# Kernel tuning notes

Hardware: AMD Instinct MI355X
Metric: run time of the kernel (lower is better)

The kernel has to match this reference:

```python
import jax, jax.numpy as jnp
import numpy as np

B, N_IN, N_MF, N_RULES, N_OUT_MEM, N_OUT = 16384, 6, 5, 2048, 12, 2
TANH_CENTERS = np.array([0.0, 0.75], dtype=np.float32)
TANH_SCALE = np.array([4.0, 0.75], dtype=np.float32)
EPS = 1e-12


def setup_inputs() -> dict:
    key = jax.random.key(0)
    k = jax.random.split(key, 6)
    x = jax.random.normal(k[0], (B, N_IN), dtype=jnp.float32)
    mf_centers = jax.random.normal(k[1], (N_IN, N_MF), dtype=jnp.float32)
    # strictly positive widths for the Gaussian memberships
    mf_scales = jax.random.uniform(k[2], (N_IN, N_MF), dtype=jnp.float32) + 0.5
    out_centers = jax.random.normal(k[3], (N_OUT_MEM,), dtype=jnp.float32)
    input_rules = jax.random.randint(k[4], (N_RULES, N_IN), 0, N_IN * N_MF, dtype=jnp.int32)
    output_rules = jax.random.randint(k[5], (N_RULES, N_OUT), 0, N_OUT_MEM, dtype=jnp.int32)
    return {"x": x, "mf_centers": mf_centers, "mf_scales": mf_scales,
            "out_centers": out_centers, "input_rules": input_rules,
            "output_rules": output_rules}


def reference(x, mf_centers, mf_scales, out_centers, input_rules, output_rules):
    # fuzzify: Gaussian membership per (input var, MF) -> [B, N_IN*N_MF]
    z = (x[:, :, None] - mf_centers[None]) / mf_scales[None]      # [B, N_IN, N_MF]
    fuzzified = jnp.exp(-z * z).reshape(x.shape[0], -1)           # [B, 30]
    # rules: gather antecedent memberships, min t-norm over antecedents
    gathered = fuzzified[:, input_rules]                          # [B, R, N_IN]
    weights = jnp.min(gathered, axis=2)                           # [B, R]
    # L1 normalize across rules (F.normalize p=1, dim=1)
    l1 = jnp.sum(jnp.abs(weights), axis=1, keepdims=True)
    normalized = weights / jnp.maximum(l1, EPS)
    # defuzzify: gather output-membership centers per rule, then matmul
    ow = out_centers[output_rules]                                # [R, N_OUT]
    defuzz = normalized @ ow                                      # [B, N_OUT]
    # constrain scaling
    return jnp.tanh(defuzz) * jnp.asarray(TANH_SCALE) + jnp.asarray(TANH_CENTERS)
```

## Files before the change

kernel.cpp:

```cpp
#include <hip/hip_runtime.h>
#include <hip/hip_bf16.h>

#define BATCH      16384
#define N_IN       6
#define N_MF       5
#define N_FUZZ     30
#define N_RULES    2048
#define N_OUT_MEM  12

#define ROWS_PB    256
#define SPLITS     4
#define RULES_PB   (N_RULES / SPLITS)
#define THREADS    1024
#define WAVES      16
#define RULES_PW   (RULES_PB / WAVES)
#define ROWGROUPS  (BATCH / ROWS_PB)

#define WS_PACKED_OFF  0
#define WS_OW_OFF      8192
#define WS_PART_OFF    24576

typedef _Float16 f16x2 __attribute__((ext_vector_type(2)));

__device__ inline int probe_is_bf16(const void* mfs) {
    const unsigned int* w = (const unsigned int*)mfs;
    int ok = 1;
    for (int k = 0; k < 15; ++k) {
        const unsigned int v = w[k];
        const float lo = __uint_as_float(v << 16);
        const float hi = __uint_as_float(v & 0xffff0000u);
        if (!(lo >= 0.4f && lo <= 1.6f && hi >= 0.4f && hi <= 1.6f)) { ok = 0; break; }
    }
    return ok;
}

__global__ void anfis_prep(const int* __restrict__ input_rules,
                           const int* __restrict__ output_rules,
                           const void* __restrict__ oc_,
                           const void* __restrict__ mfs_,
                           unsigned int* __restrict__ packed,
                           float2* __restrict__ ow) {
    __shared__ int flag;
    if (threadIdx.x == 0) flag = probe_is_bf16(mfs_);
    __syncthreads();
    const bool is_bf16 = (flag != 0);

    const int r = blockIdx.x * blockDim.x + threadIdx.x;
    if (r >= N_RULES) return;
    const int* rp = input_rules + r * N_IN;
    unsigned int p = 0;
#pragma unroll
    for (int i = 0; i < N_IN; ++i) p |= ((unsigned int)rp[i] & 31u) << (5 * i);
    packed[r] = p;

    const int o0i = output_rules[2 * r + 0];
    const int o1i = output_rules[2 * r + 1];
    float o0, o1;
    if (is_bf16) {
        const unsigned short* oc = (const unsigned short*)oc_;
        o0 = __uint_as_float((unsigned int)oc[o0i] << 16);
        o1 = __uint_as_float((unsigned int)oc[o1i] << 16);
    } else {
        const float* oc = (const float*)oc_;
        o0 = oc[o0i]; o1 = oc[o1i];
    }
    ow[r] = make_float2(o0, o1);
}

__global__ __launch_bounds__(THREADS, 4)
void anfis_main(const void* __restrict__ x_,
                const void* __restrict__ mfc_,
                const void* __restrict__ mfs_,
                const unsigned int* __restrict__ packed,
                const float2* __restrict__ ow,
                float* __restrict__ partials) {
    __shared__ float xs[ROWS_PB * N_IN];
    __shared__ float2 cinv[N_FUZZ];
    __shared__ uint2 fuzz4[N_FUZZ][64];
    __shared__ float pl1[WAVES][ROWS_PB];
    __shared__ float pd0[WAVES][ROWS_PB];
    __shared__ float pd1[WAVES][ROWS_PB];
    __shared__ int flag;

    const int t     = threadIdx.x;
    const int g     = blockIdx.x >> 2;
    const int split = blockIdx.x & 3;
    const int row0  = g * ROWS_PB;

    if (t == 0) flag = probe_is_bf16(mfs_);
    __syncthreads();
    const bool is_bf16 = (flag != 0);

    if (is_bf16) {
        const unsigned short* xp = (const unsigned short*)x_ + row0 * N_IN;
        for (int i = t; i < ROWS_PB * N_IN; i += THREADS)
            xs[i] = __uint_as_float((unsigned int)xp[i] << 16);
    } else {
        const float* xp = (const float*)x_ + row0 * N_IN;
        for (int i = t; i < ROWS_PB * N_IN; i += THREADS) xs[i] = xp[i];
    }
    if (t < N_FUZZ) {
        float c, s;
        if (is_bf16) {
            c = __uint_as_float((unsigned int)((const unsigned short*)mfc_)[t] << 16);
            s = __uint_as_float((unsigned int)((const unsigned short*)mfs_)[t] << 16);
        } else {
            c = ((const float*)mfc_)[t];
            s = ((const float*)mfs_)[t];
        }
        cinv[t] = make_float2(c, 1.0f / s);
    }
    __syncthreads();

    for (int e = t; e < N_FUZZ * 64; e += THREADS) {
        const int v    = e >> 6;
        const int lane = e & 63;
        const int i    = v / N_MF;
        const float2 ci = cinv[v];
        float f[4];
#pragma unroll
        for (int k = 0; k < 4; ++k) {
            const float z = (xs[(lane + 64 * k) * N_IN + i] - ci.x) * ci.y;
            f[k] = __expf(-z * z);
        }
        f16x2 a = { (_Float16)f[0], (_Float16)f[1] };
        f16x2 b = { (_Float16)f[2], (_Float16)f[3] };
        uint2 u;
        u.x = __builtin_bit_cast(unsigned int, a);
        u.y = __builtin_bit_cast(unsigned int, b);
        fuzz4[v][lane] = u;
    }
    __syncthreads();

    const int lane = t & 63;
    const int wave = __builtin_amdgcn_readfirstlane(t >> 6);
    const uint2* fz = &fuzz4[0][0];

    float l1[4] = {0.f, 0.f, 0.f, 0.f};
    float d0[4] = {0.f, 0.f, 0.f, 0.f};
    float d1[4] = {0.f, 0.f, 0.f, 0.f};

    const int rbase = split * RULES_PB + wave * RULES_PW;
#pragma unroll 4
    for (int j = 0; j < RULES_PW; ++j) {
        const int r = rbase + j;
        const unsigned int p = packed[r];
        const float2 o = ow[r];
        const uint2 g0 = fz[((p      ) & 31u) * 64 + lane];
        const uint2 g1 = fz[((p >> 5 ) & 31u) * 64 + lane];
        const uint2 g2 = fz[((p >> 10) & 31u) * 64 + lane];
        const uint2 g3 = fz[((p >> 15) & 31u) * 64 + lane];
        const uint2 g4 = fz[((p >> 20) & 31u) * 64 + lane];
        const uint2 g5 = fz[((p >> 25) & 31u) * 64 + lane];
        f16x2 wa = __builtin_elementwise_min(__builtin_bit_cast(f16x2, g0.x),
                                             __builtin_bit_cast(f16x2, g1.x));
        wa = __builtin_elementwise_min(wa, __builtin_bit_cast(f16x2, g2.x));
        wa = __builtin_elementwise_min(wa, __builtin_bit_cast(f16x2, g3.x));
        wa = __builtin_elementwise_min(wa, __builtin_bit_cast(f16x2, g4.x));
        wa = __builtin_elementwise_min(wa, __builtin_bit_cast(f16x2, g5.x));
        f16x2 wb = __builtin_elementwise_min(__builtin_bit_cast(f16x2, g0.y),
                                             __builtin_bit_cast(f16x2, g1.y));
        wb = __builtin_elementwise_min(wb, __builtin_bit_cast(f16x2, g2.y));
        wb = __builtin_elementwise_min(wb, __builtin_bit_cast(f16x2, g3.y));
        wb = __builtin_elementwise_min(wb, __builtin_bit_cast(f16x2, g4.y));
        wb = __builtin_elementwise_min(wb, __builtin_bit_cast(f16x2, g5.y));
        const float w0 = (float)wa.x, w1 = (float)wa.y;
        const float w2 = (float)wb.x, w3 = (float)wb.y;
        l1[0] += w0; d0[0] += w0 * o.x; d1[0] += w0 * o.y;
        l1[1] += w1; d0[1] += w1 * o.x; d1[1] += w1 * o.y;
        l1[2] += w2; d0[2] += w2 * o.x; d1[2] += w2 * o.y;
        l1[3] += w3; d0[3] += w3 * o.x; d1[3] += w3 * o.y;
    }
#pragma unroll
    for (int k = 0; k < 4; ++k) {
        pl1[wave][lane + 64 * k] = l1[k];
        pd0[wave][lane + 64 * k] = d0[k];
        pd1[wave][lane + 64 * k] = d1[k];
    }
    __syncthreads();

    if (t < ROWS_PB) {
        float a = 0.f, b = 0.f, c = 0.f;
#pragma unroll
        for (int wv = 0; wv < WAVES; ++wv) {
            a += pl1[wv][t];
            b += pd0[wv][t];
            c += pd1[wv][t];
        }
        const int row = row0 + t;
        partials[(split * 3 + 0) * BATCH + row] = a;
        partials[(split * 3 + 1) * BATCH + row] = b;
        partials[(split * 3 + 2) * BATCH + row] = c;
    }
}

__global__ void anfis_finalize(const float* __restrict__ partials,
                               const void* __restrict__ mfs_,
                               void* __restrict__ out_) {
    __shared__ int flag;
    if (threadIdx.x == 0) flag = probe_is_bf16(mfs_);
    __syncthreads();
    const int row = blockIdx.x * blockDim.x + threadIdx.x;
    if (row >= BATCH) return;
    float l1 = 0.f, d0 = 0.f, d1 = 0.f;
#pragma unroll
    for (int s = 0; s < SPLITS; ++s) {
        l1 += partials[(s * 3 + 0) * BATCH + row];
        d0 += partials[(s * 3 + 1) * BATCH + row];
        d1 += partials[(s * 3 + 2) * BATCH + row];
    }
    const float inv = 1.0f / fmaxf(l1, 1e-12f);
    const float y0 = tanhf(d0 * inv) * 4.00f + 0.00f;
    const float y1 = tanhf(d1 * inv) * 0.75f + 0.75f;
    if (flag) {
        __hip_bfloat162 o;
        o.x = __float2bfloat16(y0);
        o.y = __float2bfloat16(y1);
        ((__hip_bfloat162*)out_)[row] = o;
    } else {
        ((float2*)out_)[row] = make_float2(y0, y1);
    }
}

extern "C" void kernel_launch(void* const* d_in, const int* in_sizes, int n_in,
                              void* d_out, int out_size, void* d_ws, size_t ws_size,
                              hipStream_t stream) {
    (void)in_sizes; (void)n_in; (void)out_size; (void)ws_size;
    const void* x_   = d_in[0];
    const void* mfc_ = d_in[1];
    const void* mfs_ = d_in[2];
    const void* oc_  = d_in[3];
    const int* input_rules  = (const int*)d_in[4];
    const int* output_rules = (const int*)d_in[5];

    unsigned int* packed = (unsigned int*)((char*)d_ws + WS_PACKED_OFF);
    float2*       ow     = (float2*)((char*)d_ws + WS_OW_OFF);
    float*        parts  = (float*)((char*)d_ws + WS_PART_OFF);

    anfis_prep<<<(N_RULES + 255) / 256, 256, 0, stream>>>(
        input_rules, output_rules, oc_, mfs_, packed, ow);

    anfis_main<<<ROWGROUPS * SPLITS, THREADS, 0, stream>>>(
        x_, mfc_, mfs_, packed, ow, parts);

    anfis_finalize<<<BATCH / 256, 256, 0, stream>>>(parts, mfs_, d_out);
}
```

Baseline: 80.96 us.

## Fuse prep, main and finalize kernels using last-block atomic reduction

Merges the three launches into one kernel. Each block packs its split's rule indices and output weights into LDS, so the separate prep kernel and its global round trip go away. The last of the four split blocks for a row group, found with an atomic counter, sums the partials and applies tanh, replacing the finalize kernel. In exchange every block now redoes rule preprocessing, and the change adds a memset plus threadfence/atomic synchronisation.

```diff
diff --git a/kernel.cpp b/kernel.cpp
--- a/kernel.cpp
+++ b/kernel.cpp
@@ -16,9 +16,8 @@
 #define RULES_PW   (RULES_PB / WAVES)
 #define ROWGROUPS  (BATCH / ROWS_PB)
 
-#define WS_PACKED_OFF  0
-#define WS_OW_OFF      8192
-#define WS_PART_OFF    24576
+#define WS_PART_OFF  0
+#define WS_CNT_OFF   (SPLITS * 3 * BATCH * 4)
 
 typedef _Float16 f16x2 __attribute__((ext_vector_type(2)));
 
@@ -34,53 +33,26 @@
     return ok;
 }
 
-__global__ void anfis_prep(const int* __restrict__ input_rules,
-                           const int* __restrict__ output_rules,
-                           const void* __restrict__ oc_,
-                           const void* __restrict__ mfs_,
-                           unsigned int* __restrict__ packed,
-                           float2* __restrict__ ow) {
-    __shared__ int flag;
-    if (threadIdx.x == 0) flag = probe_is_bf16(mfs_);
-    __syncthreads();
-    const bool is_bf16 = (flag != 0);
-
-    const int r = blockIdx.x * blockDim.x + threadIdx.x;
-    if (r >= N_RULES) return;
-    const int* rp = input_rules + r * N_IN;
-    unsigned int p = 0;
-#pragma unroll
-    for (int i = 0; i < N_IN; ++i) p |= ((unsigned int)rp[i] & 31u) << (5 * i);
-    packed[r] = p;
-
-    const int o0i = output_rules[2 * r + 0];
-    const int o1i = output_rules[2 * r + 1];
-    float o0, o1;
-    if (is_bf16) {
-        const unsigned short* oc = (const unsigned short*)oc_;
-        o0 = __uint_as_float((unsigned int)oc[o0i] << 16);
-        o1 = __uint_as_float((unsigned int)oc[o1i] << 16);
-    } else {
-        const float* oc = (const float*)oc_;
-        o0 = oc[o0i]; o1 = oc[o1i];
-    }
-    ow[r] = make_float2(o0, o1);
-}
-
 __global__ __launch_bounds__(THREADS, 4)
-void anfis_main(const void* __restrict__ x_,
-                const void* __restrict__ mfc_,
-                const void* __restrict__ mfs_,
-                const unsigned int* __restrict__ packed,
-                const float2* __restrict__ ow,
-                float* __restrict__ partials) {
-    __shared__ float xs[ROWS_PB * N_IN];
-    __shared__ float2 cinv[N_FUZZ];
-    __shared__ uint2 fuzz4[N_FUZZ][64];
-    __shared__ float pl1[WAVES][ROWS_PB];
-    __shared__ float pd0[WAVES][ROWS_PB];
-    __shared__ float pd1[WAVES][ROWS_PB];
-    __shared__ int flag;
+void anfis_fused(const void* __restrict__ x_,
+                 const void* __restrict__ mfc_,
+                 const void* __restrict__ mfs_,
+                 const void* __restrict__ oc_,
+                 const int*  __restrict__ input_rules,
+                 const int*  __restrict__ output_rules,
+                 float* __restrict__ partials,
+                 int*   __restrict__ counters,
+                 void*  __restrict__ out_) {
+    __shared__ float        xs[ROWS_PB * N_IN];
+    __shared__ float2       cinv[N_FUZZ];
+    __shared__ uint2        fuzz4[N_FUZZ][64];
+    __shared__ unsigned int packed_lds[RULES_PB];
+    __shared__ float2       ow_lds[RULES_PB];
+    __shared__ float        pl1[WAVES][ROWS_PB];
+    __shared__ float        pd0[WAVES][ROWS_PB];
+    __shared__ float        pd1[WAVES][ROWS_PB];
+    __shared__ int          flag;
+    __shared__ int          amLast;
 
     const int t     = threadIdx.x;
     const int g     = blockIdx.x >> 2;
@@ -90,6 +62,27 @@
     if (t == 0) flag = probe_is_bf16(mfs_);
     __syncthreads();
     const bool is_bf16 = (flag != 0);
+
+    for (int r2 = t; r2 < RULES_PB; r2 += THREADS) {
+        const int r = split * RULES_PB + r2;
+        const int* rp = input_rules + r * N_IN;
+        unsigned int p = 0;
+#pragma unroll
+        for (int i = 0; i < N_IN; ++i) p |= ((unsigned int)rp[i] & 31u) << (5 * i);
+        packed_lds[r2] = p;
+        const int o0i = output_rules[2 * r + 0];
+        const int o1i = output_rules[2 * r + 1];
+        float o0, o1;
+        if (is_bf16) {
+            const unsigned short* oc = (const unsigned short*)oc_;
+            o0 = __uint_as_float((unsigned int)oc[o0i] << 16);
+            o1 = __uint_as_float((unsigned int)oc[o1i] << 16);
+        } else {
+            const float* oc = (const float*)oc_;
+            o0 = oc[o0i]; o1 = oc[o1i];
+        }
+        ow_lds[r2] = make_float2(o0, o1);
+    }
 
     if (is_bf16) {
         const unsigned short* xp = (const unsigned short*)x_ + row0 * N_IN;
@@ -140,12 +133,12 @@
     float d0[4] = {0.f, 0.f, 0.f, 0.f};
     float d1[4] = {0.f, 0.f, 0.f, 0.f};
 
-    const int rbase = split * RULES_PB + wave * RULES_PW;
+    const int rbase = wave * RULES_PW;
 #pragma unroll 4
     for (int j = 0; j < RULES_PW; ++j) {
-        const int r = rbase + j;
-        const unsigned int p = packed[r];
-        const float2 o = ow[r];
+        const int r2 = rbase + j;
+        const unsigned int p = packed_lds[r2];
+        const float2 o = ow_lds[r2];
         const uint2 g0 = fz[((p      ) & 31u) * 64 + lane];
         const uint2 g1 = fz[((p >> 5 ) & 31u) * 64 + lane];
         const uint2 g2 = fz[((p >> 10) & 31u) * 64 + lane];
@@ -192,33 +185,36 @@
         partials[(split * 3 + 1) * BATCH + row] = b;
         partials[(split * 3 + 2) * BATCH + row] = c;
     }
-}
-
-__global__ void anfis_finalize(const float* __restrict__ partials,
-                               const void* __restrict__ mfs_,
-                               void* __restrict__ out_) {
-    __shared__ int flag;
-    if (threadIdx.x == 0) flag = probe_is_bf16(mfs_);
-    __syncthreads();
-    const int row = blockIdx.x * blockDim.x + threadIdx.x;
-    if (row >= BATCH) return;
-    float l1 = 0.f, d0 = 0.f, d1 = 0.f;
-#pragma unroll
-    for (int s = 0; s < SPLITS; ++s) {
-        l1 += partials[(s * 3 + 0) * BATCH + row];
-        d0 += partials[(s * 3 + 1) * BATCH + row];
-        d1 += partials[(s * 3 + 2) * BATCH + row];
-    }
-    const float inv = 1.0f / fmaxf(l1, 1e-12f);
-    const float y0 = tanhf(d0 * inv) * 4.00f + 0.00f;
-    const float y1 = tanhf(d1 * inv) * 0.75f + 0.75f;
-    if (flag) {
-        __hip_bfloat162 o;
-        o.x = __float2bfloat16(y0);
-        o.y = __float2bfloat16(y1);
-        ((__hip_bfloat162*)out_)[row] = o;
-    } else {
-        ((float2*)out_)[row] = make_float2(y0, y1);
+    __threadfence();
+    if (t == 0) {
+        const int old = atomicAdd(&counters[g], 1);
+        amLast = (old == SPLITS - 1);
+    }
+    __syncthreads();
+
+    if (amLast) {
+        __threadfence();
+        if (t < ROWS_PB) {
+            const int row = row0 + t;
+            float l1s = 0.f, d0s = 0.f, d1s = 0.f;
+#pragma unroll
+            for (int s = 0; s < SPLITS; ++s) {
+                l1s += partials[(s * 3 + 0) * BATCH + row];
+                d0s += partials[(s * 3 + 1) * BATCH + row];
+                d1s += partials[(s * 3 + 2) * BATCH + row];
+            }
+            const float inv = 1.0f / fmaxf(l1s, 1e-12f);
+            const float y0 = tanhf(d0s * inv) * 4.00f + 0.00f;
+            const float y1 = tanhf(d1s * inv) * 0.75f + 0.75f;
+            if (is_bf16) {
+                __hip_bfloat162 o;
+                o.x = __float2bfloat16(y0);
+                o.y = __float2bfloat16(y1);
+                ((__hip_bfloat162*)out_)[row] = o;
+            } else {
+                ((float2*)out_)[row] = make_float2(y0, y1);
+            }
+        }
     }
 }
 
@@ -226,22 +222,13 @@
                               void* d_out, int out_size, void* d_ws, size_t ws_size,
                               hipStream_t stream) {
     (void)in_sizes; (void)n_in; (void)out_size; (void)ws_size;
-    const void* x_   = d_in[0];
-    const void* mfc_ = d_in[1];
-    const void* mfs_ = d_in[2];
-    const void* oc_  = d_in[3];
-    const int* input_rules  = (const int*)d_in[4];
-    const int* output_rules = (const int*)d_in[5];
-
-    unsigned int* packed = (unsigned int*)((char*)d_ws + WS_PACKED_OFF);
-    float2*       ow     = (float2*)((char*)d_ws + WS_OW_OFF);
-    float*        parts  = (float*)((char*)d_ws + WS_PART_OFF);
-
-    anfis_prep<<<(N_RULES + 255) / 256, 256, 0, stream>>>(
-        input_rules, output_rules, oc_, mfs_, packed, ow);
-
-    anfis_main<<<ROWGROUPS * SPLITS, THREADS, 0, stream>>>(
-        x_, mfc_, mfs_, packed, ow, parts);
-
-    anfis_finalize<<<BATCH / 256, 256, 0, stream>>>(parts, mfs_, d_out);
+    float* parts    = (float*)((char*)d_ws + WS_PART_OFF);
+    int*   counters = (int*)((char*)d_ws + WS_CNT_OFF);
+
+    hipMemsetAsync(counters, 0, ROWGROUPS * sizeof(int), stream);
+
+    anfis_fused<<<ROWGROUPS * SPLITS, THREADS, 0, stream>>>(
+        d_in[0], d_in[1], d_in[2], d_in[3],
+        (const int*)d_in[4], (const int*)d_in[5],
+        parts, counters, d_out);
 }
```

Result: slower. 166.8 us (+106.0%).
